# Kernel optimization log

Measured on AMD Instinct MI355X. Metric: run time of the kernel, lower is better.

Reference implementation:

```python
import jax, jax.numpy as jnp
import numpy as np

IN_DIM = 512        # cfg.hidden_channels
NUM_H_PATCH = 16    # cfg.num_h_patch (v_dim); also k dim after split
BASE = 10000.0      # cfg.base
OUT_DIM = IN_DIM * 2 * NUM_H_PATCH


def setup_inputs() -> dict:
    key = jax.random.key(0)
    k1, k2, k3 = jax.random.split(key, 3)
    b, n = 16, 256
    token = jax.random.normal(k1, (b, n, IN_DIM), dtype=jnp.float32)
    W_proj = jax.random.normal(k2, (IN_DIM, OUT_DIM), dtype=jnp.float32) * (IN_DIM ** -0.5)
    b_proj = jax.random.normal(k3, (OUT_DIM,), dtype=jnp.float32) * 0.01
    return {"token": token, "W_proj": W_proj, "b_proj": b_proj}


def reference(token, W_proj, b_proj):
    b, n, _ = token.shape
    d = 2 * NUM_H_PATCH
    kv = token @ W_proj + b_proj                       # [b, n, in_dim*2*num_h_patch]
    kv = kv.reshape(b, n, IN_DIM, d).transpose(0, 2, 1, 3)  # b h n d, h=in_dim
    k = kv[..., : NUM_H_PATCH]                         # [b, h, n, num_h_patch]
    v = kv[..., NUM_H_PATCH:]                          # [b, h, n, num_h_patch]
    k = jax.nn.silu(k)
    # rotary phase: theta buffer (h, 1, num_h_patch//2), index = n-1-arange(n)
    d_theta = IN_DIM * NUM_H_PATCH
    freqs = BASE ** (-2.0 / d_theta * jnp.arange(d_theta // 2, dtype=jnp.float32))
    theta = freqs.reshape(IN_DIM, 1, NUM_H_PATCH // 2)
    index = (n - 1 - jnp.arange(n, dtype=jnp.float32)).reshape(n, 1)
    ang = theta * index                                # [h, n, num_h_patch//2]
    ang = jnp.repeat(ang, 2, axis=-1)                  # '... d -> ... (d g)', g=2
    cos, sin = jnp.cos(ang), jnp.sin(ang)
    # rotate-half: interleave (-k_odd, k_even)
    k_half = jnp.stack([-k[..., 1::2], k[..., ::2]], axis=-1).reshape(k.shape)
    k = k * cos + k_half * sin
    # fast-weight memory: per-head outer-product reduction over sequence
    wm = jnp.einsum('bhnd,bhne->bdeh', k, v)           # [b, num_h_patch, num_h_patch, in_dim]
    return wm.reshape(b, NUM_H_PATCH * NUM_H_PATCH, IN_DIM)
```

## Files before the change

### kernel.cpp

```cpp
#include <hip/hip_runtime.h>
#include <hip/hip_bf16.h>

typedef __bf16 bf16;
typedef __bf16 bf16x4 __attribute__((ext_vector_type(4)));
typedef __bf16 bf16x8 __attribute__((ext_vector_type(8)));
typedef float f32x4 __attribute__((ext_vector_type(4)));

#define GLOBAL_AS __attribute__((address_space(1)))
#define LDS_AS __attribute__((address_space(3)))

__device__ __forceinline__ void gload_lds16(const void* g, void* l) {
  __builtin_amdgcn_global_load_lds((const GLOBAL_AS void*)g, (LDS_AS void*)l, 16, 0, 0);
}

__global__ __launch_bounds__(256) void cvt_token_k(const float* __restrict__ t,
                                                   bf16* __restrict__ o) {
  int base = (blockIdx.x * 256 + threadIdx.x) * 4;
  f32x4 v = *(const f32x4*)(t + base);
  bf16x4 b;
  b[0] = (bf16)v[0]; b[1] = (bf16)v[1]; b[2] = (bf16)v[2]; b[3] = (bf16)v[3];
  *(bf16x4*)(o + base) = b;
}

__global__ __launch_bounds__(256) void transpose_w_k(const float* __restrict__ w,
                                                     bf16* __restrict__ wt) {
  __shared__ float tile[32][33];
  int j0 = blockIdx.x * 32;
  int k0 = blockIdx.y * 32;
  int tx = threadIdx.x & 31;
  int ty = threadIdx.x >> 5;
#pragma unroll
  for (int i = 0; i < 4; ++i)
    tile[ty + i * 8][tx] = w[(size_t)(k0 + ty + i * 8) * 16384 + j0 + tx];
  __syncthreads();
#pragma unroll
  for (int i = 0; i < 4; ++i)
    wt[(size_t)(j0 + ty + i * 8) * 512 + k0 + tx] = (bf16)tile[tx][ty + i * 8];
}

__global__ __launch_bounds__(512, 2) void fused_main_k(
    const bf16* __restrict__ A, const bf16* __restrict__ Wt,
    const float* __restrict__ bias, float* __restrict__ out) {
  __shared__ char smem[65536];
  const int tid = threadIdx.x;
  const int lane = tid & 63;
  const int w = tid >> 6;
  const int wr = w >> 1;
  const int wc = w & 1;
  const int b = blockIdx.y;
  const int hg = blockIdx.x;
  const int m0 = b << 8;
  const int j0 = hg << 7;

  f32x4 acc[4][4] = {};

  for (int ks = 0; ks < 8; ++ks) {
    const int kbase = ks << 6;
#pragma unroll
    for (int i = 0; i < 4; ++i) {
      int q = (i * 8 + w) * 64 + lane;
      int r = q >> 3;
      int cc = (q & 7) ^ (r & 7);
      gload_lds16(A + (size_t)(m0 + r) * 512 + kbase + cc * 8,
                  smem + (i * 8 + w) * 1024);
    }
#pragma unroll
    for (int i = 0; i < 2; ++i) {
      int q = (i * 8 + w) * 64 + lane;
      int r = q >> 3;
      int cc = (q & 7) ^ (r & 7);
      gload_lds16(Wt + (size_t)(j0 + r) * 512 + kbase + cc * 8,
                  smem + 32768 + (i * 8 + w) * 1024);
    }
    __syncthreads();
#pragma unroll
    for (int kk = 0; kk < 2; ++kk) {
      const int cbyte = (kk * 32 + (lane >> 4) * 8) * 2;
      bf16x8 af[4], bfr[4];
#pragma unroll
      for (int mf = 0; mf < 4; ++mf) {
        int r = wr * 64 + mf * 16 + (lane & 15);
        af[mf] = *(const bf16x8*)(smem + r * 128 + (cbyte ^ ((r & 7) << 4)));
      }
#pragma unroll
      for (int nf = 0; nf < 4; ++nf) {
        int r = wc * 64 + nf * 16 + (lane & 15);
        bfr[nf] = *(const bf16x8*)(smem + 32768 + r * 128 + (cbyte ^ ((r & 7) << 4)));
      }
#pragma unroll
      for (int mf = 0; mf < 4; ++mf)
#pragma unroll
        for (int nf = 0; nf < 4; ++nf)
          acc[mf][nf] = __builtin_amdgcn_mfma_f32_16x16x32_bf16(
              af[mf], bfr[nf], acc[mf][nf], 0, 0, 0);
    }
    __syncthreads();
  }

#pragma unroll
  for (int nf = 0; nf < 4; ++nf) {
    const int col = wc * 64 + nf * 16 + (lane & 15);
    const int hl = col >> 5;
    const int dd = lane & 15;
    const bool isk = ((nf & 1) == 0);
    const float bv = bias[j0 + col];
    float freq = 0.f, sgn = 0.f;
    if (isk) {
      const int t = dd >> 1;
      const int hglob = (hg << 2) + hl;
      freq = exp2f((float)(hglob * 8 + t) * (-13.287712379549449f / 4096.0f));
      sgn = (dd & 1) ? 1.0f : -1.0f;
    }
#pragma unroll
    for (int mf = 0; mf < 4; ++mf) {
      const int n0 = wr * 64 + mf * 16 + ((lane >> 4) << 2);
      f32x4 c = acc[mf][nf];
#pragma unroll
      for (int j = 0; j < 4; ++j) {
        float x = c[j] + bv;
        if (isk) x = x * __builtin_amdgcn_rcpf(1.0f + __expf(-x));
        c[j] = x;
      }
      if (isk) {
#pragma unroll
        for (int j = 0; j < 4; ++j) {
          float partner = __shfl_xor(c[j], 1);
          float sv, cv;
          __sincosf(freq * (float)(255 - (n0 + j)), &sv, &cv);
          c[j] = c[j] * cv + sgn * partner * sv;
        }
      }
      bf16x4 pk;
      pk[0] = (bf16)c[0]; pk[1] = (bf16)c[1]; pk[2] = (bf16)c[2]; pk[3] = (bf16)c[3];
      int byte = (isk ? 0 : 32768) + hl * 8192 + dd * 512 + n0 * 2;
      byte ^= ((dd & 7) << 4);
      *(bf16x4*)(smem + byte) = pk;
    }
  }
  __syncthreads();

  {
    const int hl = w >> 1;
    const int half = w & 1;
    const int dd = lane & 15;
    f32x4 d2 = {0.f, 0.f, 0.f, 0.f};
#pragma unroll
    for (int kk = 0; kk < 4; ++kk) {
      const int n0 = half * 128 + kk * 32 + ((lane >> 4) << 3);
      int byte = hl * 8192 + dd * 512 + n0 * 2;
      byte ^= ((dd & 7) << 4);
      bf16x8 ka = *(const bf16x8*)(smem + byte);
      bf16x8 vb = *(const bf16x8*)(smem + 32768 + byte);
      d2 = __builtin_amdgcn_mfma_f32_16x16x32_bf16(ka, vb, d2, 0, 0, 0);
    }
    __syncthreads();
    float* part = (float*)smem;
#pragma unroll
    for (int j = 0; j < 4; ++j) {
      int de = (((lane >> 4) << 2) + j) * 16 + dd;
      part[w * 256 + de] = d2[j];
    }
  }
  __syncthreads();

  if (tid < 256) {
    const float* part = (const float*)smem;
    f32x4 o;
#pragma unroll
    for (int hl = 0; hl < 4; ++hl)
      o[hl] = part[(2 * hl) * 256 + tid] + part[(2 * hl + 1) * 256 + tid];
    *(f32x4*)(out + (size_t)b * 131072 + (size_t)tid * 512 + hg * 4) = o;
  }
}

extern "C" void kernel_launch(void* const* d_in, const int* in_sizes, int n_in,
                              void* d_out, int out_size, void* d_ws, size_t ws_size,
                              hipStream_t stream) {
  const float* token = (const float*)d_in[0];
  const float* W     = (const float*)d_in[1];
  const float* bias  = (const float*)d_in[2];
  float* out = (float*)d_out;

  bf16* Abf = (bf16*)d_ws;
  bf16* Wt  = (bf16*)((char*)d_ws + (size_t)4 * 1024 * 1024);

  cvt_token_k<<<2048, 256, 0, stream>>>(token, Abf);
  transpose_w_k<<<dim3(512, 16), 256, 0, stream>>>(W, Wt);
  fused_main_k<<<dim3(128, 16), 512, 0, stream>>>(Abf, Wt, bias, out);
}
```

Before: 93.99 us.

## Triple-buffer GEMM K-loop with async LDS prefetch and MFMA priority

Replaces the single-buffered K loop, which loads then syncs then computes, with a three-stage LDS ring. Each stage is prefetched two steps ahead using global_load_lds, and fine-grained vmcnt waits replace full syncthreads. Wave priority is raised around the MFMA block. LDS grows to 144KB per block, which limits occupancy to one block per CU despite the launch bound requesting two.

```diff
diff --git a/kernel.cpp b/kernel.cpp
--- a/kernel.cpp
+++ b/kernel.cpp
@@ -41,7 +41,7 @@
 __global__ __launch_bounds__(512, 2) void fused_main_k(
     const bf16* __restrict__ A, const bf16* __restrict__ Wt,
     const float* __restrict__ bias, float* __restrict__ out) {
-  __shared__ char smem[65536];
+  __shared__ char smem[147456];
   const int tid = threadIdx.x;
   const int lane = tid & 63;
   const int w = tid >> 6;
@@ -54,47 +54,87 @@
 
   f32x4 acc[4][4] = {};
 
-  for (int ks = 0; ks < 8; ++ks) {
-    const int kbase = ks << 6;
+#pragma unroll
+  for (int t = 0; t < 2; ++t) {
+    const int base = t * 49152;
+    const int kb = t << 6;
 #pragma unroll
     for (int i = 0; i < 4; ++i) {
       int q = (i * 8 + w) * 64 + lane;
       int r = q >> 3;
       int cc = (q & 7) ^ (r & 7);
-      gload_lds16(A + (size_t)(m0 + r) * 512 + kbase + cc * 8,
-                  smem + (i * 8 + w) * 1024);
+      gload_lds16(A + (size_t)(m0 + r) * 512 + kb + cc * 8,
+                  smem + base + (i * 8 + w) * 1024);
     }
 #pragma unroll
     for (int i = 0; i < 2; ++i) {
       int q = (i * 8 + w) * 64 + lane;
       int r = q >> 3;
       int cc = (q & 7) ^ (r & 7);
-      gload_lds16(Wt + (size_t)(j0 + r) * 512 + kbase + cc * 8,
-                  smem + 32768 + (i * 8 + w) * 1024);
-    }
-    __syncthreads();
+      gload_lds16(Wt + (size_t)(j0 + r) * 512 + kb + cc * 8,
+                  smem + base + 32768 + (i * 8 + w) * 1024);
+    }
+  }
+  asm volatile("s_waitcnt vmcnt(6)" ::: "memory");
+  __builtin_amdgcn_s_barrier();
+  asm volatile("" ::: "memory");
+
+#pragma unroll
+  for (int t = 0; t < 8; ++t) {
+    const int cbase = (t % 3) * 49152;
+    const int nbase = ((t + 2) % 3) * 49152;
+    const int kb2 = (t + 2) << 6;
+    if (t < 6) {
+#pragma unroll
+      for (int i = 0; i < 4; ++i) {
+        int q = (i * 8 + w) * 64 + lane;
+        int r = q >> 3;
+        int cc = (q & 7) ^ (r & 7);
+        gload_lds16(A + (size_t)(m0 + r) * 512 + kb2 + cc * 8,
+                    smem + nbase + (i * 8 + w) * 1024);
+      }
+    }
 #pragma unroll
     for (int kk = 0; kk < 2; ++kk) {
+      if (kk == 1 && t < 6) {
+#pragma unroll
+        for (int i = 0; i < 2; ++i) {
+          int q = (i * 8 + w) * 64 + lane;
+          int r = q >> 3;
+          int cc = (q & 7) ^ (r & 7);
+          gload_lds16(Wt + (size_t)(j0 + r) * 512 + kb2 + cc * 8,
+                      smem + nbase + 32768 + (i * 8 + w) * 1024);
+        }
+      }
       const int cbyte = (kk * 32 + (lane >> 4) * 8) * 2;
       bf16x8 af[4], bfr[4];
 #pragma unroll
       for (int mf = 0; mf < 4; ++mf) {
         int r = wr * 64 + mf * 16 + (lane & 15);
-        af[mf] = *(const bf16x8*)(smem + r * 128 + (cbyte ^ ((r & 7) << 4)));
+        af[mf] = *(const bf16x8*)(smem + cbase + r * 128 + (cbyte ^ ((r & 7) << 4)));
       }
 #pragma unroll
       for (int nf = 0; nf < 4; ++nf) {
         int r = wc * 64 + nf * 16 + (lane & 15);
-        bfr[nf] = *(const bf16x8*)(smem + 32768 + r * 128 + (cbyte ^ ((r & 7) << 4)));
-      }
+        bfr[nf] = *(const bf16x8*)(smem + cbase + 32768 + r * 128 + (cbyte ^ ((r & 7) << 4)));
+      }
+      __builtin_amdgcn_s_setprio(1);
 #pragma unroll
       for (int mf = 0; mf < 4; ++mf)
 #pragma unroll
         for (int nf = 0; nf < 4; ++nf)
           acc[mf][nf] = __builtin_amdgcn_mfma_f32_16x16x32_bf16(
               af[mf], bfr[nf], acc[mf][nf], 0, 0, 0);
-    }
-    __syncthreads();
+      __builtin_amdgcn_s_setprio(0);
+    }
+    asm volatile("" ::: "memory");
+    if (t < 6) {
+      asm volatile("s_waitcnt vmcnt(6)" ::: "memory");
+    } else if (t == 6) {
+      asm volatile("s_waitcnt vmcnt(0)" ::: "memory");
+    }
+    __builtin_amdgcn_s_barrier();
+    asm volatile("" ::: "memory");
   }
 
 #pragma unroll
```

Measured after the change: 111.9 us. 1.19x slower.

## Triple-buffer GEMM K-loop with async LDS loads and vmcnt-based barriers

Applied to the files above, without the earlier changes.

Restructures the GEMM main loop of the fused kernel from single-buffered 64-wide K steps with two syncthreads per step into a 3-stage ring of 32-wide K tiles. Global-to-LDS loads for step t+2 are issued before computing step t, and synchronisation uses a partial s_waitcnt vmcnt plus a single s_barrier. It also uses a new pair-row swizzled LDS layout, raises MFMA priority with s_setprio, and changes launch bounds to target 4 blocks. The aim is to hide global-load latency behind MFMA work, at the cost of more LDS (72KB) and the risk of register pressure from the higher occupancy target.

```diff
diff --git a/kernel.cpp b/kernel.cpp
--- a/kernel.cpp
+++ b/kernel.cpp
@@ -38,10 +38,10 @@
     wt[(size_t)(j0 + ty + i * 8) * 512 + k0 + tx] = (bf16)tile[tx][ty + i * 8];
 }
 
-__global__ __launch_bounds__(512, 2) void fused_main_k(
+__global__ __launch_bounds__(512, 4) void fused_main_k(
     const bf16* __restrict__ A, const bf16* __restrict__ Wt,
     const float* __restrict__ bias, float* __restrict__ out) {
-  __shared__ char smem[65536];
+  __shared__ char smem[73728];
   const int tid = threadIdx.x;
   const int lane = tid & 63;
   const int w = tid >> 6;
@@ -52,49 +52,89 @@
   const int m0 = b << 8;
   const int j0 = hg << 7;
 
+  int rA[2], kA[2];
+#pragma unroll
+  for (int i = 0; i < 2; ++i) {
+    int c = i * 512 + tid;
+    int rp = c >> 3, half = (c >> 2) & 1, slot = c & 3;
+    rA[i] = rp * 2 + half;
+    kA[i] = (slot ^ (rp & 3)) << 3;
+  }
+  int rB, kB;
+  {
+    int c = tid;
+    int rp = c >> 3, half = (c >> 2) & 1, slot = c & 3;
+    rB = rp * 2 + half;
+    kB = (slot ^ (rp & 3)) << 3;
+  }
+
+  int offA[4], offB[4];
+#pragma unroll
+  for (int mf = 0; mf < 4; ++mf) {
+    int r = wr * 64 + mf * 16 + (lane & 15);
+    int rp = r >> 1;
+    offA[mf] = rp * 128 + (r & 1) * 64 + ((((lane >> 4)) ^ (rp & 3)) << 4);
+  }
+#pragma unroll
+  for (int nf = 0; nf < 4; ++nf) {
+    int cjj = wc * 64 + nf * 16 + (lane & 15);
+    int rp = cjj >> 1;
+    offB[nf] = rp * 128 + (cjj & 1) * 64 + ((((lane >> 4)) ^ (rp & 3)) << 4);
+  }
+
   f32x4 acc[4][4] = {};
 
-  for (int ks = 0; ks < 8; ++ks) {
-    const int kbase = ks << 6;
-#pragma unroll
-    for (int i = 0; i < 4; ++i) {
-      int q = (i * 8 + w) * 64 + lane;
-      int r = q >> 3;
-      int cc = (q & 7) ^ (r & 7);
-      gload_lds16(A + (size_t)(m0 + r) * 512 + kbase + cc * 8,
-                  smem + (i * 8 + w) * 1024);
-    }
-#pragma unroll
-    for (int i = 0; i < 2; ++i) {
-      int q = (i * 8 + w) * 64 + lane;
-      int r = q >> 3;
-      int cc = (q & 7) ^ (r & 7);
-      gload_lds16(Wt + (size_t)(j0 + r) * 512 + kbase + cc * 8,
-                  smem + 32768 + (i * 8 + w) * 1024);
-    }
-    __syncthreads();
-#pragma unroll
-    for (int kk = 0; kk < 2; ++kk) {
-      const int cbyte = (kk * 32 + (lane >> 4) * 8) * 2;
-      bf16x8 af[4], bfr[4];
-#pragma unroll
-      for (int mf = 0; mf < 4; ++mf) {
-        int r = wr * 64 + mf * 16 + (lane & 15);
-        af[mf] = *(const bf16x8*)(smem + r * 128 + (cbyte ^ ((r & 7) << 4)));
-      }
-#pragma unroll
-      for (int nf = 0; nf < 4; ++nf) {
-        int r = wc * 64 + nf * 16 + (lane & 15);
-        bfr[nf] = *(const bf16x8*)(smem + 32768 + r * 128 + (cbyte ^ ((r & 7) << 4)));
-      }
-#pragma unroll
-      for (int mf = 0; mf < 4; ++mf)
-#pragma unroll
-        for (int nf = 0; nf < 4; ++nf)
-          acc[mf][nf] = __builtin_amdgcn_mfma_f32_16x16x32_bf16(
-              af[mf], bfr[nf], acc[mf][nf], 0, 0, 0);
-    }
-    __syncthreads();
+#pragma unroll
+  for (int t = 0; t < 2; ++t) {
+    const int nb = t * 24576;
+    const int kb = t << 5;
+#pragma unroll
+    for (int i = 0; i < 2; ++i)
+      gload_lds16(A + (size_t)(m0 + rA[i]) * 512 + kb + kA[i],
+                  smem + nb + (i * 8 + w) * 1024);
+    gload_lds16(Wt + (size_t)(j0 + rB) * 512 + kb + kB,
+                smem + nb + 16384 + w * 1024);
+  }
+  asm volatile("s_waitcnt vmcnt(3)" ::: "memory");
+  __builtin_amdgcn_s_barrier();
+  asm volatile("" ::: "memory");
+
+#pragma unroll
+  for (int t = 0; t < 16; ++t) {
+    const int cb = (t % 3) * 24576;
+    if (t < 14) {
+      const int nb = ((t + 2) % 3) * 24576;
+      const int kb2 = (t + 2) << 5;
+#pragma unroll
+      for (int i = 0; i < 2; ++i)
+        gload_lds16(A + (size_t)(m0 + rA[i]) * 512 + kb2 + kA[i],
+                    smem + nb + (i * 8 + w) * 1024);
+      gload_lds16(Wt + (size_t)(j0 + rB) * 512 + kb2 + kB,
+                  smem + nb + 16384 + w * 1024);
+    }
+    bf16x8 af[4], bfr[4];
+#pragma unroll
+    for (int mf = 0; mf < 4; ++mf)
+      af[mf] = *(const bf16x8*)(smem + cb + offA[mf]);
+#pragma unroll
+    for (int nf = 0; nf < 4; ++nf)
+      bfr[nf] = *(const bf16x8*)(smem + cb + 16384 + offB[nf]);
+    __builtin_amdgcn_s_setprio(1);
+#pragma unroll
+    for (int mf = 0; mf < 4; ++mf)
+#pragma unroll
+      for (int nf = 0; nf < 4; ++nf)
+        acc[mf][nf] = __builtin_amdgcn_mfma_f32_16x16x32_bf16(
+            af[mf], bfr[nf], acc[mf][nf], 0, 0, 0);
+    __builtin_amdgcn_s_setprio(0);
+    asm volatile("" ::: "memory");
+    if (t < 14) {
+      asm volatile("s_waitcnt vmcnt(3)" ::: "memory");
+    } else if (t == 14) {
+      asm volatile("s_waitcnt vmcnt(0)" ::: "memory");
+    }
+    __builtin_amdgcn_s_barrier();
+    asm volatile("" ::: "memory");
   }
 
 #pragma unroll
```

After: 96.63 us. 1.03x slower.

## Enlarge GEMM tile to 256x256 with double-buffered async LDS pipeline

Applied to the files above, without the earlier changes.

The fused kernel now gives each block a 256-column slice (8 heads) instead of 128, which halves the grid and doubles A-tile reuse. The K loop uses 128 KB of LDS, double-buffered in half-K sub-stages. Global-to-LDS loads are issued between MFMA phases, with explicit vmcnt waits, raw barriers and setprio. The epilogue reduction is reworked so each wave handles one head over the full sequence, and all 512 threads write the output. The larger LDS footprint limits occupancy to one block per CU and fewer blocks, and the hand-counted waits risk races if the counts are wrong.

```diff
diff --git a/kernel.cpp b/kernel.cpp
--- a/kernel.cpp
+++ b/kernel.cpp
@@ -12,6 +12,10 @@
 __device__ __forceinline__ void gload_lds16(const void* g, void* l) {
   __builtin_amdgcn_global_load_lds((const GLOBAL_AS void*)g, (LDS_AS void*)l, 16, 0, 0);
 }
+
+#define PHASE_BAR() do { asm volatile("" ::: "memory"); \
+    __builtin_amdgcn_s_barrier(); asm volatile("" ::: "memory"); } while (0)
+#define WAITV(n) asm volatile("s_waitcnt vmcnt(" #n ")" ::: "memory")
 
 __global__ __launch_bounds__(256) void cvt_token_k(const float* __restrict__ t,
                                                    bf16* __restrict__ o) {
@@ -41,79 +45,145 @@
 __global__ __launch_bounds__(512, 2) void fused_main_k(
     const bf16* __restrict__ A, const bf16* __restrict__ Wt,
     const float* __restrict__ bias, float* __restrict__ out) {
-  __shared__ char smem[65536];
+  __shared__ char smem[131072];
   const int tid = threadIdx.x;
   const int lane = tid & 63;
   const int w = tid >> 6;
-  const int wr = w >> 1;
-  const int wc = w & 1;
+  const int wm = w >> 2;
+  const int wn = w & 3;
   const int b = blockIdx.y;
   const int hg = blockIdx.x;
   const int m0 = b << 8;
-  const int j0 = hg << 7;
-
-  f32x4 acc[4][4] = {};
-
-  for (int ks = 0; ks < 8; ++ks) {
-    const int kbase = ks << 6;
-#pragma unroll
-    for (int i = 0; i < 4; ++i) {
-      int q = (i * 8 + w) * 64 + lane;
-      int r = q >> 3;
-      int cc = (q & 7) ^ (r & 7);
-      gload_lds16(A + (size_t)(m0 + r) * 512 + kbase + cc * 8,
-                  smem + (i * 8 + w) * 1024);
-    }
-#pragma unroll
-    for (int i = 0; i < 2; ++i) {
-      int q = (i * 8 + w) * 64 + lane;
-      int r = q >> 3;
-      int cc = (q & 7) ^ (r & 7);
-      gload_lds16(Wt + (size_t)(j0 + r) * 512 + kbase + cc * 8,
-                  smem + 32768 + (i * 8 + w) * 1024);
-    }
-    __syncthreads();
-#pragma unroll
-    for (int kk = 0; kk < 2; ++kk) {
-      const int cbyte = (kk * 32 + (lane >> 4) * 8) * 2;
-      bf16x8 af[4], bfr[4];
-#pragma unroll
-      for (int mf = 0; mf < 4; ++mf) {
-        int r = wr * 64 + mf * 16 + (lane & 15);
-        af[mf] = *(const bf16x8*)(smem + r * 128 + (cbyte ^ ((r & 7) << 4)));
-      }
-#pragma unroll
-      for (int nf = 0; nf < 4; ++nf) {
-        int r = wc * 64 + nf * 16 + (lane & 15);
-        bfr[nf] = *(const bf16x8*)(smem + 32768 + r * 128 + (cbyte ^ ((r & 7) << 4)));
-      }
-#pragma unroll
-      for (int mf = 0; mf < 4; ++mf)
-#pragma unroll
-        for (int nf = 0; nf < 4; ++nf)
-          acc[mf][nf] = __builtin_amdgcn_mfma_f32_16x16x32_bf16(
-              af[mf], bfr[nf], acc[mf][nf], 0, 0, 0);
-    }
-    __syncthreads();
-  }
-
+  const int j0 = hg << 8;
+
+  int rS[2], kS[2];
+#pragma unroll
+  for (int i = 0; i < 2; ++i) {
+    int c = i * 512 + tid;
+    rS[i] = c >> 2;
+    kS[i] = ((c & 3) ^ ((rS[i] >> 1) & 3)) << 3;
+  }
+  const bf16* Abase = A + (size_t)m0 * 512;
+  const bf16* Bbase = Wt + (size_t)j0 * 512;
+
+  int offA[2][4], offB[4];
+#pragma unroll
+  for (int mh = 0; mh < 2; ++mh)
+#pragma unroll
+    for (int q = 0; q < 4; ++q) {
+      int r = wm * 128 + mh * 64 + q * 16 + (lane & 15);
+      offA[mh][q] = r * 64 + (((lane >> 4) ^ ((r >> 1) & 3)) << 4);
+    }
 #pragma unroll
   for (int nf = 0; nf < 4; ++nf) {
-    const int col = wc * 64 + nf * 16 + (lane & 15);
-    const int hl = col >> 5;
+    int r = wn * 64 + nf * 16 + (lane & 15);
+    offB[nf] = r * 64 + (((lane >> 4) ^ ((r >> 1) & 3)) << 4);
+  }
+
+#define STAGE_A(t_, kk_, d_) do { \
+    gload_lds16(Abase + (size_t)rS[0]*512 + ((t_)<<6) + ((kk_)<<5) + kS[0], \
+                smem + ((d_)*2 + (kk_))*16384 + (w*64)*16); \
+    gload_lds16(Abase + (size_t)rS[1]*512 + ((t_)<<6) + ((kk_)<<5) + kS[1], \
+                smem + ((d_)*2 + (kk_))*16384 + (512 + w*64)*16); \
+  } while (0)
+#define STAGE_B(t_, kk_, d_) do { \
+    gload_lds16(Bbase + (size_t)rS[0]*512 + ((t_)<<6) + ((kk_)<<5) + kS[0], \
+                smem + 65536 + ((d_)*2 + (kk_))*16384 + (w*64)*16); \
+    gload_lds16(Bbase + (size_t)rS[1]*512 + ((t_)<<6) + ((kk_)<<5) + kS[1], \
+                smem + 65536 + ((d_)*2 + (kk_))*16384 + (512 + w*64)*16); \
+  } while (0)
+
+  f32x4 acc[8][4] = {};
+
+  STAGE_A(0, 0, 0); STAGE_B(0, 0, 0);
+  STAGE_A(0, 1, 0); STAGE_B(0, 1, 0);
+  STAGE_A(1, 0, 1); STAGE_B(1, 0, 1);
+  WAITV(8);
+  PHASE_BAR();
+
+#pragma unroll
+  for (int t = 0; t < 8; ++t) {
+    const int d = t & 1;
+    const char* Ak0 = smem + (d * 2 + 0) * 16384;
+    const char* Ak1 = smem + (d * 2 + 1) * 16384;
+    const char* Bk0 = smem + 65536 + (d * 2 + 0) * 16384;
+    const char* Bk1 = smem + 65536 + (d * 2 + 1) * 16384;
+    bf16x8 af[4], bfr[4];
+
+#pragma unroll
+    for (int nf = 0; nf < 4; ++nf) bfr[nf] = *(const bf16x8*)(Bk0 + offB[nf]);
+#pragma unroll
+    for (int q = 0; q < 4; ++q) af[q] = *(const bf16x8*)(Ak0 + offA[0][q]);
+    if (t + 1 < 8) STAGE_A(t + 1, 1, d ^ 1);
+    __builtin_amdgcn_s_setprio(1);
+#pragma unroll
+    for (int q = 0; q < 4; ++q)
+#pragma unroll
+      for (int nf = 0; nf < 4; ++nf)
+        acc[q][nf] = __builtin_amdgcn_mfma_f32_16x16x32_bf16(af[q], bfr[nf], acc[q][nf], 0, 0, 0);
+    __builtin_amdgcn_s_setprio(0);
+    PHASE_BAR();
+
+#pragma unroll
+    for (int q = 0; q < 4; ++q) af[q] = *(const bf16x8*)(Ak0 + offA[1][q]);
+    if (t + 1 < 8) STAGE_B(t + 1, 1, d ^ 1);
+    __builtin_amdgcn_s_setprio(1);
+#pragma unroll
+    for (int q = 0; q < 4; ++q)
+#pragma unroll
+      for (int nf = 0; nf < 4; ++nf)
+        acc[4 + q][nf] = __builtin_amdgcn_mfma_f32_16x16x32_bf16(af[q], bfr[nf], acc[4 + q][nf], 0, 0, 0);
+    __builtin_amdgcn_s_setprio(0);
+    if (t == 7) { WAITV(0); } else { WAITV(8); }
+    PHASE_BAR();
+
+#pragma unroll
+    for (int nf = 0; nf < 4; ++nf) bfr[nf] = *(const bf16x8*)(Bk1 + offB[nf]);
+#pragma unroll
+    for (int q = 0; q < 4; ++q) af[q] = *(const bf16x8*)(Ak1 + offA[0][q]);
+    if (t + 2 < 8) STAGE_A(t + 2, 0, d);
+    __builtin_amdgcn_s_setprio(1);
+#pragma unroll
+    for (int q = 0; q < 4; ++q)
+#pragma unroll
+      for (int nf = 0; nf < 4; ++nf)
+        acc[q][nf] = __builtin_amdgcn_mfma_f32_16x16x32_bf16(af[q], bfr[nf], acc[q][nf], 0, 0, 0);
+    __builtin_amdgcn_s_setprio(0);
+    PHASE_BAR();
+
+#pragma unroll
+    for (int q = 0; q < 4; ++q) af[q] = *(const bf16x8*)(Ak1 + offA[1][q]);
+    if (t + 2 < 8) STAGE_B(t + 2, 0, d);
+    __builtin_amdgcn_s_setprio(1);
+#pragma unroll
+    for (int q = 0; q < 4; ++q)
+#pragma unroll
+      for (int nf = 0; nf < 4; ++nf)
+        acc[4 + q][nf] = __builtin_amdgcn_mfma_f32_16x16x32_bf16(af[q], bfr[nf], acc[4 + q][nf], 0, 0, 0);
+    __builtin_amdgcn_s_setprio(0);
+    if (t < 6) { WAITV(8); } else if (t == 6) { WAITV(4); }
+    PHASE_BAR();
+  }
+#undef STAGE_A
+#undef STAGE_B
+
+#pragma unroll
+  for (int nf = 0; nf < 4; ++nf) {
+    const int col = wn * 64 + nf * 16 + (lane & 15);
+    const int chl = col >> 5;
     const int dd = lane & 15;
     const bool isk = ((nf & 1) == 0);
     const float bv = bias[j0 + col];
     float freq = 0.f, sgn = 0.f;
     if (isk) {
-      const int t = dd >> 1;
-      const int hglob = (hg << 2) + hl;
-      freq = exp2f((float)(hglob * 8 + t) * (-13.287712379549449f / 4096.0f));
+      const int tp = dd >> 1;
+      const int chg = (hg << 3) + chl;
+      freq = exp2f((float)(chg * 8 + tp) * (-13.287712379549449f / 4096.0f));
       sgn = (dd & 1) ? 1.0f : -1.0f;
     }
 #pragma unroll
-    for (int mf = 0; mf < 4; ++mf) {
-      const int n0 = wr * 64 + mf * 16 + ((lane >> 4) << 2);
+    for (int mf = 0; mf < 8; ++mf) {
+      const int n0 = wm * 128 + mf * 16 + ((lane >> 4) << 2);
       f32x4 c = acc[mf][nf];
 #pragma unroll
       for (int j = 0; j < 4; ++j) {
@@ -132,7 +202,7 @@
       }
       bf16x4 pk;
       pk[0] = (bf16)c[0]; pk[1] = (bf16)c[1]; pk[2] = (bf16)c[2]; pk[3] = (bf16)c[3];
-      int byte = (isk ? 0 : 32768) + hl * 8192 + dd * 512 + n0 * 2;
+      int byte = (isk ? 0 : 65536) + chl * 8192 + dd * 512 + n0 * 2;
       byte ^= ((dd & 7) << 4);
       *(bf16x4*)(smem + byte) = pk;
     }
@@ -140,17 +210,15 @@
   __syncthreads();
 
   {
-    const int hl = w >> 1;
-    const int half = w & 1;
     const int dd = lane & 15;
     f32x4 d2 = {0.f, 0.f, 0.f, 0.f};
 #pragma unroll
-    for (int kk = 0; kk < 4; ++kk) {
-      const int n0 = half * 128 + kk * 32 + ((lane >> 4) << 3);
-      int byte = hl * 8192 + dd * 512 + n0 * 2;
+    for (int kk2 = 0; kk2 < 8; ++kk2) {
+      const int n0 = kk2 * 32 + ((lane >> 4) << 3);
+      int byte = w * 8192 + dd * 512 + n0 * 2;
       byte ^= ((dd & 7) << 4);
       bf16x8 ka = *(const bf16x8*)(smem + byte);
-      bf16x8 vb = *(const bf16x8*)(smem + 32768 + byte);
+      bf16x8 vb = *(const bf16x8*)(smem + 65536 + byte);
       d2 = __builtin_amdgcn_mfma_f32_16x16x32_bf16(ka, vb, d2, 0, 0, 0);
     }
     __syncthreads();
@@ -158,18 +226,16 @@
 #pragma unroll
     for (int j = 0; j < 4; ++j) {
       int de = (((lane >> 4) << 2) + j) * 16 + dd;
-      part[w * 256 + de] = d2[j];
+      part[de * 8 + w] = d2[j];
     }
   }
   __syncthreads();
 
-  if (tid < 256) {
+  {
     const float* part = (const float*)smem;
-    f32x4 o;
-#pragma unroll
-    for (int hl = 0; hl < 4; ++hl)
-      o[hl] = part[(2 * hl) * 256 + tid] + part[(2 * hl + 1) * 256 + tid];
-    *(f32x4*)(out + (size_t)b * 131072 + (size_t)tid * 512 + hg * 4) = o;
+    int de = tid >> 1, c4 = (tid & 1) << 2;
+    f32x4 o = *(const f32x4*)(part + de * 8 + c4);
+    *(f32x4*)(out + (size_t)b * 131072 + (size_t)de * 512 + (hg << 3) + c4) = o;
   }
 }
 
@@ -186,5 +252,5 @@
 
   cvt_token_k<<<2048, 256, 0, stream>>>(token, Abf);
   transpose_w_k<<<dim3(512, 16), 256, 0, stream>>>(W, Wt);
-  fused_main_k<<<dim3(128, 16), 512, 0, stream>>>(Abf, Wt, bias, out);
-}
+  fused_main_k<<<dim3(64, 16), 512, 0, stream>>>(Abf, Wt, bias, out);
+}
```

After: 101.8 us. 8.3% more time.
